# Kernel optimization log

Hardware: AMD Instinct MI355X
Metric: run time of the kernel (lower is better)

Reference implementation:

```python
import jax, jax.numpy as jnp
import numpy as np

N_NODES = 100000
N_HE = 20000
N_INC = 800000
D = 128
HEADS = 4
OUT = D // HEADS  # 32
NEG_SLOPE = 0.2
EPS_GN = 1e-5
EPS_SM = 1e-16


def graph_norm(x, w, b, ms):
    # PyG GraphNorm over a single graph: subtract learnable-scaled mean, normalize by std
    mean = jnp.mean(x, axis=0, keepdims=True)
    xc = x - ms * mean
    var = jnp.mean(xc * xc, axis=0, keepdims=True)
    return w * xc / jnp.sqrt(var + EPS_GN) + b


def frame_update(x, eidx, eattr, W, att, bias):
    # x: [N, D], eidx: [2, E] (row0 node ids, row1 hyperedge ids), eattr: [HE, D]
    xh = (x @ W).reshape(-1, HEADS, OUT)       # [N, H, O]
    eh = (eattr @ W).reshape(-1, HEADS, OUT)   # [HE, H, O]
    src = eidx[0]
    dst = eidx[1]
    x_i = xh[src]                              # [E, H, O] gathered node feats
    x_j = eh[dst]                              # [E, H, O] gathered hyperedge feats
    # attention logit: cat([x_i, x_j]) . att  summed over feature dim
    alpha = jnp.sum(x_i * att[:, :, :OUT], axis=-1) + jnp.sum(x_j * att[:, :, OUT:], axis=-1)  # [E, H]
    alpha = jnp.where(alpha >= 0, alpha, NEG_SLOPE * alpha)  # leaky_relu
    # segment softmax grouped by hyperedge id (dst), num_segments = N_HE
    m = jax.ops.segment_max(alpha, dst, num_segments=N_HE)   # [HE, H]
    ex = jnp.exp(alpha - m[dst])
    s = jax.ops.segment_sum(ex, dst, num_segments=N_HE)      # [HE, H]
    alpha = ex / (s[dst] + EPS_SM)                           # [E, H]
    # message = alpha * x_j where propagate's x_j = x[edge_index[0]] (node feats)
    msg = alpha[:, :, None] * x_i                            # [E, H, O]
    out = jax.ops.segment_sum(msg, dst, num_segments=N_HE)   # [HE, H, O]
    out = out.reshape(-1, HEADS * OUT)                       # concat heads
    return out + bias


def setup_inputs() -> dict:
    key = jax.random.key(0)
    ks = jax.random.split(key, 12)
    g = 1.0 / np.sqrt(D)
    inp = {
        "intra_x": jax.random.normal(ks[0], (N_NODES, D), jnp.float32),
        "intra_edge_attr": jax.random.normal(ks[1], (N_HE, D), jnp.float32),
        "inter_x": jax.random.normal(ks[2], (N_NODES, D), jnp.float32),
        "inter_edge_attr": jax.random.normal(ks[3], (N_HE, D), jnp.float32),
        "intra_edge_index": jnp.stack([
            jax.random.randint(ks[4], (N_INC,), 0, N_NODES),
            jax.random.randint(ks[5], (N_INC,), 0, N_HE)]).astype(jnp.int32),
        "inter_edge_index": jnp.stack([
            jax.random.randint(ks[6], (N_INC,), 0, N_NODES),
            jax.random.randint(ks[7], (N_INC,), 0, N_HE)]).astype(jnp.int32),
        "gn_intra_w": jnp.ones((D,), jnp.float32),
        "gn_intra_b": jnp.zeros((D,), jnp.float32),
        "gn_intra_ms": jnp.ones((D,), jnp.float32),
        "W_intra": jax.random.normal(ks[8], (D, HEADS * OUT), jnp.float32) * g,
        "att_intra": jax.random.normal(ks[9], (1, HEADS, 2 * OUT), jnp.float32) * g,
        "b_intra": jnp.zeros((HEADS * OUT,), jnp.float32),
        "gn_inter_w": jnp.ones((D,), jnp.float32),
        "gn_inter_b": jnp.zeros((D,), jnp.float32),
        "gn_inter_ms": jnp.ones((D,), jnp.float32),
        "W_inter": jax.random.normal(ks[10], (D, HEADS * OUT), jnp.float32) * g,
        "att_inter": jax.random.normal(ks[11], (1, HEADS, 2 * OUT), jnp.float32) * g,
        "b_inter": jnp.zeros((HEADS * OUT,), jnp.float32),
    }
    return inp


def reference(intra_x, intra_edge_index, intra_edge_attr,
              inter_x, inter_edge_index, inter_edge_attr,
              gn_intra_w, gn_intra_b, gn_intra_ms, W_intra, att_intra, b_intra,
              gn_inter_w, gn_inter_b, gn_inter_ms, W_inter, att_inter, b_inter):
    f_intra = frame_update(graph_norm(intra_x, gn_intra_w, gn_intra_b, gn_intra_ms),
                           intra_edge_index, intra_edge_attr, W_intra, att_intra, b_intra)
    f_inter = frame_update(graph_norm(inter_x, gn_inter_w, gn_inter_b, gn_inter_ms),
                           inter_edge_index, inter_edge_attr, W_inter, att_inter, b_inter)
    fusion = jnp.concatenate([
        jnp.mean(f_intra, axis=0),
        jnp.mean(f_inter, axis=0),
        jnp.mean(intra_x, axis=0),
        jnp.mean(inter_x, axis=0),
    ], axis=-1)  # [4*D]
    return fusion
```

## Files before the change

kernel.cpp:

```cpp
#include <hip/hip_runtime.h>

#define N_NODES 100000
#define N_HE    20000
#define N_EDGE  800000
#define DIM     128
#define NBS     98
#define NBD     40
#define CAP_S   9600
#define CAP_D   22500
#define SUBS    8
#define SUBD    16
#define PB      256
#define CHUNK   3125
#define STB     400
#define GPB     512
#define GGRP    32

struct P {
  const void* x[2]; const void* ea[2]; const int* ei[2];
  const void* gw[2]; const void* gb[2]; const void* gms[2];
  const void* W[2]; const void* att[2]; const void* bias[2];
  float *stats, *a, *cw, *v, *u, *cst, *sPart, *wnPart, *gpart, *gpart2;
  unsigned *curS, *curD, *recS, *recD, *done;
  unsigned short *lnb, *lhb, *hsv;
  int* flag; void* out;
};

__device__ __forceinline__ float ldf(const void* p, int i, int isbf){
  if (isbf){ unsigned short h = ((const unsigned short*)p)[i]; return __uint_as_float(((unsigned)h)<<16); }
  return ((const float*)p)[i];
}
__device__ __forceinline__ float b2f(unsigned short h){
  return __uint_as_float(((unsigned)h)<<16);
}
struct F8 { float v[8]; };
__device__ __forceinline__ F8 load8(const void* p, long idx, int isbf){
  F8 r;
  if (isbf){
    uint4 q = *(const uint4*)((const unsigned short*)p + idx);
    r.v[0]=__uint_as_float(q.x<<16); r.v[1]=__uint_as_float(q.x&0xFFFF0000u);
    r.v[2]=__uint_as_float(q.y<<16); r.v[3]=__uint_as_float(q.y&0xFFFF0000u);
    r.v[4]=__uint_as_float(q.z<<16); r.v[5]=__uint_as_float(q.z&0xFFFF0000u);
    r.v[6]=__uint_as_float(q.w<<16); r.v[7]=__uint_as_float(q.w&0xFFFF0000u);
  } else {
    const float4* q = (const float4*)((const float*)p + idx);
    float4 A=q[0], B=q[1];
    r.v[0]=A.x;r.v[1]=A.y;r.v[2]=A.z;r.v[3]=A.w;
    r.v[4]=B.x;r.v[5]=B.y;r.v[6]=B.z;r.v[7]=B.w;
  }
  return r;
}
__device__ __forceinline__ unsigned short f2bf(float f){
  unsigned u = __float_as_uint(f);
  return (unsigned short)((u + 0x7FFFu + ((u>>16)&1u)) >> 16);
}

__global__ void k_detect(P p){
  for (int i=threadIdx.x; i<880; i+=256) p.stats[i]=0.f;
  const unsigned* w = (const unsigned*)p.x[0];
  int bad = 0;
  for (int i = threadIdx.x; i < 4096; i += 256){
    float g = __uint_as_float(w[i]<<16);
    float ag = fabsf(g);
    if (!(ag==0.0f || (ag>1e-8f && ag<1e8f))) bad++;
  }
  for (int o=32;o;o>>=1) bad += __shfl_down(bad,o);
  __shared__ int sb;
  if (threadIdx.x==0) sb=0;
  __syncthreads();
  if ((threadIdx.x&63)==0) atomicAdd(&sb,bad);
  __syncthreads();
  if (threadIdx.x==0) *p.flag = (sb < 512) ? 1 : 0;
}

__global__ __launch_bounds__(256) void k_statsbin(P p){
  __shared__ unsigned smem[6664];
  int t = threadIdx.x;
  if (blockIdx.y < 2){
    int f = blockIdx.y;
    const void* x = p.x[f];
    int isbf = *p.flag;
    int cb = t & 15, rg = t >> 4;
    int rpb = (N_NODES + STB - 1)/STB;
    int r0 = blockIdx.x*rpb;
    int r1 = r0 + rpb; if (r1 > N_NODES) r1 = N_NODES;
    float s[8], q[8];
    #pragma unroll
    for (int j=0;j<8;j++){ s[j]=0.f; q[j]=0.f; }
    for (int r = r0 + rg; r < r1; r += 16){
      F8 xv = load8(x, (long)r*DIM + cb*8, isbf);
      #pragma unroll
      for (int j=0;j<8;j++){ s[j]+=xv.v[j]; q[j]+=xv.v[j]*xv.v[j]; }
    }
    float* red = (float*)smem;
    #pragma unroll
    for (int j=0;j<8;j++) red[t*9+j]=s[j];
    __syncthreads();
    if (t < 128){
      int cb2 = t>>3, j = t&7;
      float a=0.f;
      for (int g=0; g<16; g++) a += red[(g*16+cb2)*9 + j];
      atomicAdd(&p.stats[f*256 + cb2*8 + j], a);
    }
    __syncthreads();
    #pragma unroll
    for (int j=0;j<8;j++) red[t*9+j]=q[j];
    __syncthreads();
    if (t < 128){
      int cb2 = t>>3, j = t&7;
      float a=0.f;
      for (int g=0; g<16; g++) a += red[(g*16+cb2)*9 + j];
      atomicAdd(&p.stats[f*256 + 128 + cb2*8 + j], a);
    }
    return;
  }
  int b = blockIdx.x, f = blockIdx.y - 2;
  if (b >= PB) return;
  unsigned* stage1 = smem;
  unsigned* stage2 = smem + 3125;
  unsigned* histS  = smem + 6250;
  unsigned* histD  = smem + 6348;
  unsigned* startS = smem + 6388;
  unsigned* startD = smem + 6486;
  unsigned* gbaseS = smem + 6526;
  unsigned* gbaseD = smem + 6624;
  const int* ei = p.ei[f];
  if (t < NBS) histS[t]=0;
  if (t < NBD) histD[t]=0;
  __syncthreads();
  int e0 = b*CHUNK;
  for (int i=t; i<CHUNK; i+=256){
    int src = ei[e0+i], dst = ei[N_EDGE+e0+i];
    unsigned nbs = (unsigned)src >> 10;
    stage1[i] = ((unsigned)src & 1023u) | ((unsigned)dst<<10) | (nbs<<25);
    atomicAdd(&histS[nbs], 1u);
    atomicAdd(&histD[(unsigned)dst>>9], 1u);
  }
  __syncthreads();
  if (t==0){ unsigned r=0; for (int k=0;k<NBS;k++){ startS[k]=r; r+=histS[k]; } }
  if (t==1){ unsigned r=0; for (int k=0;k<NBD;k++){ startD[k]=r; r+=histD[k]; } }
  __syncthreads();
  if (t < NBS) gbaseS[t] = atomicAdd(&p.curS[f*NBS+t], histS[t]);
  if (t >= 128 && t < 128+NBD) gbaseD[t-128] = atomicAdd(&p.curD[f*NBD+(t-128)], histD[t-128]);
  __syncthreads();
  if (t < NBS) histS[t]=0;
  __syncthreads();
  for (int i=t; i<CHUNK; i+=256){
    unsigned rec = stage1[i];
    unsigned nbs = rec>>25;
    unsigned r = atomicAdd(&histS[nbs],1u);
    stage2[startS[nbs]+r] = rec;
  }
  __syncthreads();
  for (int i=t; i<CHUNK; i+=256){
    unsigned rec = stage2[i];
    unsigned nbs = rec>>25;
    unsigned g = gbaseS[nbs] + (i - startS[nbs]);
    if (g < CAP_S) p.recS[((long)f*NBS+nbs)*CAP_S + g] = rec & 0x01FFFFFFu;
  }
  __syncthreads();
  if (t < NBD) histD[t]=0;
  __syncthreads();
  for (int i=t; i<CHUNK; i+=256){
    unsigned rec = stage1[i];
    unsigned dst = (rec>>10)&0x7FFFu;
    unsigned src = (rec>>25)*1024u + (rec&1023u);
    unsigned nbd = dst>>9;
    unsigned rd = (dst&511u) | (src<<9) | (nbd<<26);
    unsigned r = atomicAdd(&histD[nbd],1u);
    stage2[startD[nbd]+r] = rd;
  }
  __syncthreads();
  for (int i=t; i<CHUNK; i+=256){
    unsigned rd = stage2[i];
    unsigned nbd = rd>>26;
    unsigned g = gbaseD[nbd] + (i - startD[nbd]);
    if (g < CAP_D) p.recD[((long)f*NBD+nbd)*CAP_D + g] = rd & 0x03FFFFFFu;
  }
}

__global__ void k_prep(P p){
  __shared__ float csh[2][128];
  int t = threadIdx.x;
  int isbf = *p.flag;
  int f = t>>7, d = t&127;
  float sum = p.stats[f*256+d], sq = p.stats[f*256+128+d];
  float mean = sum * (1.0f/N_NODES);
  float ms = ldf(p.gms[f], d, isbf);
  float gw = ldf(p.gw[f],  d, isbf);
  float gb = ldf(p.gb[f],  d, isbf);
  float var = sq*(1.0f/N_NODES) - (2.0f*ms - ms*ms)*mean*mean;
  float av = gw / sqrtf(var + 1e-5f);
  p.a[f*128+d] = av;
  csh[f][d] = gb - av*ms*mean;
  if (isbf) ((unsigned short*)p.out)[256 + f*128 + d] = f2bf(mean);
  else      ((float*)p.out)[256 + f*128 + d] = mean;
  #pragma unroll
  for (int h=0; h<4; h++){
    float w1=0.f, w2=0.f;
    for (int o=0;o<32;o++){
      float Wv = ldf(p.W[f], d*DIM + h*32 + o, isbf);
      w1 += Wv * ldf(p.att[f], h*64+o,    isbf);
      w2 += Wv * ldf(p.att[f], h*64+32+o, isbf);
    }
    p.v[f*512 + d*4 + h] = av*w1;
    p.u[f*512 + d*4 + h] = w2;
  }
  __syncthreads();
  float acc = 0.f;
  for (int dd=0; dd<128; dd++) acc += csh[f][dd]*ldf(p.W[f], dd*DIM+d, isbf);
  p.cw[f*128+d] = acc;
  __syncthreads();
  if (t < 8){
    int ff=t>>2, h=t&3;
    float s2=0.f;
    for (int o=0;o<32;o++) s2 += p.cw[ff*128+h*32+o]*ldf(p.att[ff], h*64+o, isbf);
    p.cst[ff*4+h]=s2;
  }
}

__global__ __launch_bounds__(256) void k_logits(P p){
  int job = blockIdx.y;
  int f = job & 1;
  bool node = job < 2;
  int isbf = *p.flag;
  const void* X = node ? p.x[f] : p.ea[f];
  const float* coef = node ? (p.v + f*512) : (p.u + f*512);
  ushort4* outb = node ? ((ushort4*)p.lnb + (long)f*N_NODES)
                       : ((ushort4*)p.lhb + (long)f*N_HE);
  int R = node ? N_NODES : N_HE;
  int cb = threadIdx.x & 15, rl = threadIdx.x >> 4;
  float cf[8][4];
  #pragma unroll
  for (int j=0;j<8;j++)
    #pragma unroll
    for (int h=0;h<4;h++)
      cf[j][h] = coef[(cb*8+j)*4+h];
  float4 cst4 = make_float4(0.f,0.f,0.f,0.f);
  if (node) cst4 = *(const float4*)(p.cst + f*4);
  int rpb = (R + gridDim.x - 1)/gridDim.x;
  int r0 = blockIdx.x*rpb;
  int r1 = r0+rpb; if (r1>R) r1=R;
  for (int r = r0 + rl; r < r1; r += 16){
    F8 xv = load8(X, (long)r*DIM + cb*8, isbf);
    float a0=0.f,a1=0.f,a2=0.f,a3=0.f;
    #pragma unroll
    for (int j=0;j<8;j++){
      a0 += xv.v[j]*cf[j][0];
      a1 += xv.v[j]*cf[j][1];
      a2 += xv.v[j]*cf[j][2];
      a3 += xv.v[j]*cf[j][3];
    }
    #pragma unroll
    for (int m=1;m<16;m<<=1){
      a0 += __shfl_xor(a0,m);
      a1 += __shfl_xor(a1,m);
      a2 += __shfl_xor(a2,m);
      a3 += __shfl_xor(a3,m);
    }
    if (cb==0){
      ushort4 o;
      o.x = f2bf(a0 + cst4.x);
      o.y = f2bf(a1 + cst4.y);
      o.z = f2bf(a2 + cst4.z);
      o.w = f2bf(a3 + cst4.w);
      outb[r] = o;
    }
  }
}

__global__ __launch_bounds__(256) void k_sD(P p){
  __shared__ float sh[512*4];
  int nbd = blockIdx.x, sub = blockIdx.y, f = blockIdx.z, t = threadIdx.x;
  for (int i=t; i<512; i+=256) *(float4*)(sh+i*4) = make_float4(0,0,0,0);
  __syncthreads();
  unsigned cnt = p.curD[f*NBD+nbd]; if (cnt > CAP_D) cnt = CAP_D;
  int lo = (int)((long)cnt*sub/SUBD), hi = (int)((long)cnt*(sub+1)/SUBD);
  const unsigned* base = p.recD + ((long)f*NBD+nbd)*CAP_D;
  const ushort4* lnb = (const ushort4*)p.lnb + (long)f*N_NODES;
  const ushort4* lhb = (const ushort4*)p.lhb + (long)f*N_HE;
  for (int i=lo+t; i<hi; i+=256){
    unsigned rd = base[i];
    unsigned dstRel = rd & 511u;
    unsigned src = rd >> 9;
    ushort4 A = lnb[src];
    ushort4 B = lhb[nbd*512 + dstRel];
    float z0=b2f(A.x)+b2f(B.x), z1=b2f(A.y)+b2f(B.y);
    float z2=b2f(A.z)+b2f(B.z), z3=b2f(A.w)+b2f(B.w);
    z0 = z0>=0.f? z0 : 0.2f*z0;  z1 = z1>=0.f? z1 : 0.2f*z1;
    z2 = z2>=0.f? z2 : 0.2f*z2;  z3 = z3>=0.f? z3 : 0.2f*z3;
    float* tgt = sh + dstRel*4;
    atomicAdd(tgt+0, __expf(z0));
    atomicAdd(tgt+1, __expf(z1));
    atomicAdd(tgt+2, __expf(z2));
    atomicAdd(tgt+3, __expf(z3));
  }
  __syncthreads();
  float* out = p.sPart + (((long)f*NBD+nbd)*SUBD + sub)*2048;
  for (int i=t; i<512; i+=256) *(float4*)(out+i*4) = *(float4*)(sh+i*4);
}

__global__ void k_sred(P p){
  int idx = blockIdx.x*256 + threadIdx.x;
  if (idx >= 2*N_HE) return;
  int f = idx / N_HE, he = idx % N_HE;
  int nbd = he>>9, rel = he&511;
  float4 acc = make_float4(0,0,0,0);
  const float* base = p.sPart + ((long)(f*NBD+nbd)*SUBD)*2048 + rel*4;
  #pragma unroll
  for (int s=0;s<SUBD;s++){
    float4 v = *(const float4*)(base + (long)s*2048);
    acc.x+=v.x; acc.y+=v.y; acc.z+=v.z; acc.w+=v.w;
  }
  ushort4 lh = ((const ushort4*)p.lhb)[(long)f*N_HE + he];
  uint4 o;
  o.x = (unsigned)lh.x | ((unsigned)lh.y<<16);
  o.y = (unsigned)lh.z | ((unsigned)lh.w<<16);
  o.z = (unsigned)f2bf(1.0f/(acc.x+1e-16f)) | ((unsigned)f2bf(1.0f/(acc.y+1e-16f))<<16);
  o.w = (unsigned)f2bf(1.0f/(acc.z+1e-16f)) | ((unsigned)f2bf(1.0f/(acc.w+1e-16f))<<16);
  ((uint4*)p.hsv)[(long)f*N_HE + he] = o;
}

__global__ __launch_bounds__(256) void k_wnD(P p){
  __shared__ float sh[1024*4];
  int nbs = blockIdx.x, sub = blockIdx.y, f = blockIdx.z, t = threadIdx.x;
  for (int i=t; i<1024; i+=256) *(float4*)(sh+i*4) = make_float4(0,0,0,0);
  __syncthreads();
  unsigned cnt = p.curS[f*NBS+nbs]; if (cnt > CAP_S) cnt = CAP_S;
  int lo = (int)((long)cnt*sub/SUBS), hi = (int)((long)cnt*(sub+1)/SUBS);
  const unsigned* base = p.recS + ((long)f*NBS+nbs)*CAP_S;
  const ushort4* lnb = (const ushort4*)p.lnb + (long)f*N_NODES;
  const uint4* hsv = (const uint4*)p.hsv + (long)f*N_HE;
  for (int i=lo+t; i<hi; i+=256){
    unsigned rec = base[i];
    unsigned srcRel = rec & 1023u;
    unsigned dst = rec >> 10;
    ushort4 A = lnb[nbs*1024 + srcRel];
    uint4 H = hsv[dst];
    float z0=b2f(A.x)+b2f((unsigned short)(H.x&0xFFFF)), z1=b2f(A.y)+b2f((unsigned short)(H.x>>16));
    float z2=b2f(A.z)+b2f((unsigned short)(H.y&0xFFFF)), z3=b2f(A.w)+b2f((unsigned short)(H.y>>16));
    z0 = z0>=0.f? z0 : 0.2f*z0;  z1 = z1>=0.f? z1 : 0.2f*z1;
    z2 = z2>=0.f? z2 : 0.2f*z2;  z3 = z3>=0.f? z3 : 0.2f*z3;
    float si0=b2f((unsigned short)(H.z&0xFFFF)), si1=b2f((unsigned short)(H.z>>16));
    float si2=b2f((unsigned short)(H.w&0xFFFF)), si3=b2f((unsigned short)(H.w>>16));
    float* tgt = sh + srcRel*4;
    atomicAdd(tgt+0, __expf(z0)*si0);
    atomicAdd(tgt+1, __expf(z1)*si1);
    atomicAdd(tgt+2, __expf(z2)*si2);
    atomicAdd(tgt+3, __expf(z3)*si3);
  }
  __syncthreads();
  float* out = p.wnPart + (((long)f*NBS+nbs)*SUBS + sub)*4096;
  for (int i=t; i<1024; i+=256) *(float4*)(out+i*4) = *(float4*)(sh+i*4);
}

__global__ __launch_bounds__(256) void k_gpass(P p){
  int f = blockIdx.y;
  int isbf = *p.flag;
  const void* xs = p.x[f];
  int cb = threadIdx.x & 15, rg = threadIdx.x >> 4;
  float acc[8][4]; float sw[4]={0.f,0.f,0.f,0.f};
  #pragma unroll
  for (int j=0;j<8;j++)
    #pragma unroll
    for (int h=0;h<4;h++) acc[j][h]=0.f;
  int rpb = (N_NODES + gridDim.x - 1)/gridDim.x;
  int r0 = blockIdx.x*rpb;
  int r1 = r0+rpb; if (r1>N_NODES) r1=N_NODES;
  for (int r = r0 + rg; r < r1; r += 16){
    int nbs = r>>10, rel = r&1023;
    const float* wb = p.wnPart + ((long)(f*NBS+nbs)*SUBS)*4096 + rel*4;
    float4 wv = make_float4(0,0,0,0);
    #pragma unroll
    for (int s=0;s<SUBS;s++){
      float4 v = *(const float4*)(wb + (long)s*4096);
      wv.x+=v.x; wv.y+=v.y; wv.z+=v.z; wv.w+=v.w;
    }
    F8 xv = load8(xs, (long)r*DIM + cb*8, isbf);
    float wvv[4]={wv.x,wv.y,wv.z,wv.w};
    #pragma unroll
    for (int j=0;j<8;j++)
      #pragma unroll
      for (int h=0;h<4;h++) acc[j][h] += xv.v[j]*wvv[h];
    if (cb==0){ sw[0]+=wv.x; sw[1]+=wv.y; sw[2]+=wv.z; sw[3]+=wv.w; }
  }
  __shared__ float red[16][16][33];
  __shared__ float red2[16][4];
  #pragma unroll
  for (int j=0;j<8;j++)
    #pragma unroll
    for (int h=0;h<4;h++) red[rg][cb][j*4+h]=acc[j][h];
  if (cb==0){ red2[rg][0]=sw[0]; red2[rg][1]=sw[1]; red2[rg][2]=sw[2]; red2[rg][3]=sw[3]; }
  __syncthreads();
  float* gp = p.gpart + ((long)f*GPB + blockIdx.x)*520;
  for (int idx=threadIdx.x; idx<512; idx+=256){
    int d=idx>>2, h=idx&3, cb2=d>>3, j=d&7;
    float a=0.f;
    #pragma unroll
    for (int g=0; g<16; g++) a += red[g][cb2][j*4+h];
    gp[idx] = a;
  }
  if (threadIdx.x<4){
    float a=0.f;
    for (int g=0;g<16;g++) a+=red2[g][threadIdx.x];
    gp[512+threadIdx.x] = a;
  }
}

__global__ void k_gredfin(P p){
  int g = blockIdx.x, f = blockIdx.y;
  int slabs = GPB/GGRP;
  const float* base = p.gpart + ((long)f*GPB + (long)g*slabs)*520;
  for (int i=threadIdx.x; i<516; i+=256){
    float acc = 0.f;
    for (int s=0;s<slabs;s++) acc += base[(long)s*520 + i];
    p.gpart2[((long)f*GGRP + g)*520 + i] = acc;
  }
  __syncthreads();
  __threadfence();
  __shared__ unsigned isLast;
  if (threadIdx.x==0){
    unsigned old = atomicAdd(p.done, 1u);
    isLast = (old == (unsigned)(GGRP*2 - 1)) ? 1u : 0u;
  }
  __syncthreads();
  if (!isLast) return;
  __threadfence();
  __shared__ float Gs[2][512];
  __shared__ float SWs[2][4];
  int t = threadIdx.x;
  for (int idx=t; idx<2*516; idx+=256){
    int ff = idx/516, i = idx%516;
    const float* b = p.gpart2 + (long)ff*GGRP*520 + i;
    float acc = 0.f;
    for (int gg=0; gg<GGRP; gg++) acc += b[(long)gg*520];
    if (i < 512) Gs[ff][i] = acc; else SWs[ff][i-512] = acc;
  }
  __syncthreads();
  int isbf = *p.flag;
  int ff = t>>7, k = t&127, h = k>>5;
  float acc = 0.f;
  for (int d=0; d<128; d++)
    acc += Gs[ff][d*4+h] * p.a[ff*128+d] * ldf(p.W[ff], d*DIM+k, isbf);
  acc += p.cw[ff*128+k]*SWs[ff][h];
  float o = acc*(1.0f/N_HE) + ldf(p.bias[ff], k, isbf);
  if (isbf) ((unsigned short*)p.out)[ff*128+k] = f2bf(o);
  else      ((float*)p.out)[ff*128+k] = o;
}

extern "C" void kernel_launch(void* const* d_in, const int* in_sizes, int n_in,
                              void* d_out, int out_size, void* d_ws, size_t ws_size,
                              hipStream_t stream){
  P p;
  p.x[0]=d_in[0];  p.ea[0]=d_in[1];  p.x[1]=d_in[2];  p.ea[1]=d_in[3];
  p.ei[0]=(const int*)d_in[4];  p.ei[1]=(const int*)d_in[5];
  p.gw[0]=d_in[6];  p.gb[0]=d_in[7];  p.gms[0]=d_in[8];
  p.W[0]=d_in[9];   p.att[0]=d_in[10]; p.bias[0]=d_in[11];
  p.gw[1]=d_in[12]; p.gb[1]=d_in[13]; p.gms[1]=d_in[14];
  p.W[1]=d_in[15];  p.att[1]=d_in[16]; p.bias[1]=d_in[17];

  float* w = (float*)d_ws;
  size_t off = 0;
  p.stats = w+off; off += 512;
  p.flag  = (int*)(w+off); off += 8;
  p.curS  = (unsigned*)(w+off); off += 256;
  p.curD  = (unsigned*)(w+off); off += 96;
  p.done  = (unsigned*)(w+off); off += 8;
  p.a     = w+off; off += 256;
  p.cw    = w+off; off += 256;
  p.v     = w+off; off += 1024;
  p.u     = w+off; off += 1024;
  p.cst   = w+off; off += 16;
  p.lnb   = (unsigned short*)(w+off); off += (size_t)2*N_NODES*2;
  p.lhb   = (unsigned short*)(w+off); off += (size_t)2*N_HE*2;
  p.hsv   = (unsigned short*)(w+off); off += (size_t)2*N_HE*4;
  p.recS  = (unsigned*)(w+off); off += (size_t)2*NBS*CAP_S;
  p.recD  = (unsigned*)(w+off); off += (size_t)2*NBD*CAP_D;
  p.sPart = w+off; off += (size_t)2*NBD*SUBD*2048;
  p.wnPart= w+off; off += (size_t)2*NBS*SUBS*4096;
  p.gpart = w+off; off += (size_t)2*GPB*520;
  p.gpart2= w+off; off += (size_t)2*GGRP*520;
  p.out   = d_out;

  k_detect  <<<dim3(1),          dim3(256), 0, stream>>>(p);
  k_statsbin<<<dim3(STB,4),      dim3(256), 0, stream>>>(p);
  k_prep    <<<dim3(1),          dim3(256), 0, stream>>>(p);
  k_logits  <<<dim3(STB,4),      dim3(256), 0, stream>>>(p);
  k_sD      <<<dim3(NBD,SUBD,2), dim3(256), 0, stream>>>(p);
  k_sred    <<<dim3((2*N_HE+255)/256), dim3(256), 0, stream>>>(p);
  k_wnD     <<<dim3(NBS,SUBS,2), dim3(256), 0, stream>>>(p);
  k_gpass   <<<dim3(GPB,2),      dim3(256), 0, stream>>>(p);
  k_gredfin <<<dim3(GGRP,2),     dim3(256), 0, stream>>>(p);
}
```

Before: 227.2 us.

## Fuse partial reductions via last-block pattern and add coalesced fp32 streaming paths

```diff
diff --git a/kernel.cpp b/kernel.cpp
--- a/kernel.cpp
+++ b/kernel.cpp
@@ -20,8 +20,8 @@
   const void* x[2]; const void* ea[2]; const int* ei[2];
   const void* gw[2]; const void* gb[2]; const void* gms[2];
   const void* W[2]; const void* att[2]; const void* bias[2];
-  float *stats, *a, *cw, *v, *u, *cst, *sPart, *wnPart, *gpart, *gpart2;
-  unsigned *curS, *curD, *recS, *recD, *done;
+  float *stats, *a, *cw, *v, *u, *cst, *sPart, *wnPart, *wn, *gpart, *gpart2;
+  unsigned *curS, *curD, *done, *sDone, *wDone, *recS, *recD;
   unsigned short *lnb, *lhb, *hsv;
   int* flag; void* out;
 };
@@ -56,7 +56,7 @@
 }
 
 __global__ void k_detect(P p){
-  for (int i=threadIdx.x; i<880; i+=256) p.stats[i]=0.f;
+  for (int i=threadIdx.x; i<1200; i+=256) p.stats[i]=0.f;
   const unsigned* w = (const unsigned*)p.x[0];
   int bad = 0;
   for (int i = threadIdx.x; i < 4096; i += 256){
@@ -78,8 +78,39 @@
   int t = threadIdx.x;
   if (blockIdx.y < 2){
     int f = blockIdx.y;
+    int isbf = *p.flag;
+    if (!isbf){
+      const float4* xf = (const float4*)p.x[f];
+      const long NF4 = (long)N_NODES*32;
+      const long G = (long)STB*256;
+      long i0 = (long)blockIdx.x*256 + t;
+      float s0=0,s1=0,s2=0,s3=0,q0=0,q1=0,q2=0,q3=0;
+      for (long i=i0; i<NF4; i+=G){
+        float4 v = xf[i];
+        s0+=v.x; q0+=v.x*v.x; s1+=v.y; q1+=v.y*v.y;
+        s2+=v.z; q2+=v.z*v.z; s3+=v.w; q3+=v.w*v.w;
+      }
+      s0 += __shfl_xor(s0,32); q0 += __shfl_xor(q0,32);
+      s1 += __shfl_xor(s1,32); q1 += __shfl_xor(q1,32);
+      s2 += __shfl_xor(s2,32); q2 += __shfl_xor(q2,32);
+      s3 += __shfl_xor(s3,32); q3 += __shfl_xor(q3,32);
+      float* redf = (float*)smem;
+      int wave=t>>6, lane=t&63;
+      if (lane<32){
+        float* d = redf + (wave*32+lane)*8;
+        d[0]=s0; d[1]=s1; d[2]=s2; d[3]=s3; d[4]=q0; d[5]=q1; d[6]=q2; d[7]=q3;
+      }
+      __syncthreads();
+      if (t < 128){
+        int g = t>>2, k = t&3;
+        float a = redf[(0*32+g)*8+k]+redf[(1*32+g)*8+k]+redf[(2*32+g)*8+k]+redf[(3*32+g)*8+k];
+        float aq= redf[(0*32+g)*8+4+k]+redf[(1*32+g)*8+4+k]+redf[(2*32+g)*8+4+k]+redf[(3*32+g)*8+4+k];
+        atomicAdd(&p.stats[f*256 + t], a);
+        atomicAdd(&p.stats[f*256 + 128 + t], aq);
+      }
+      return;
+    }
     const void* x = p.x[f];
-    int isbf = *p.flag;
     int cb = t & 15, rg = t >> 4;
     int rpb = (N_NODES + STB - 1)/STB;
     int r0 = blockIdx.x*rpb;
@@ -88,7 +119,7 @@
     #pragma unroll
     for (int j=0;j<8;j++){ s[j]=0.f; q[j]=0.f; }
     for (int r = r0 + rg; r < r1; r += 16){
-      F8 xv = load8(x, (long)r*DIM + cb*8, isbf);
+      F8 xv = load8(x, (long)r*DIM + cb*8, 1);
       #pragma unroll
       for (int j=0;j<8;j++){ s[j]+=xv.v[j]; q[j]+=xv.v[j]*xv.v[j]; }
     }
@@ -229,20 +260,58 @@
   ushort4* outb = node ? ((ushort4*)p.lnb + (long)f*N_NODES)
                        : ((ushort4*)p.lhb + (long)f*N_HE);
   int R = node ? N_NODES : N_HE;
-  int cb = threadIdx.x & 15, rl = threadIdx.x >> 4;
+  int t = threadIdx.x;
+  float4 cst4 = make_float4(0.f,0.f,0.f,0.f);
+  if (node) cst4 = *(const float4*)(p.cst + f*4);
+  if (!isbf){
+    int c = t & 31;
+    float cf[4][4];
+    #pragma unroll
+    for (int k=0;k<4;k++)
+      #pragma unroll
+      for (int h=0;h<4;h++)
+        cf[k][h] = coef[(c*4+k)*4+h];
+    const float4* Xf = (const float4*)X;
+    const long NF4 = (long)R*32;
+    const long G = (long)gridDim.x*256;
+    long i0 = (long)blockIdx.x*256 + t;
+    for (long i=i0; i<NF4; i+=G){
+      float4 v = Xf[i];
+      float p0 = v.x*cf[0][0]+v.y*cf[1][0]+v.z*cf[2][0]+v.w*cf[3][0];
+      float p1 = v.x*cf[0][1]+v.y*cf[1][1]+v.z*cf[2][1]+v.w*cf[3][1];
+      float p2 = v.x*cf[0][2]+v.y*cf[1][2]+v.z*cf[2][2]+v.w*cf[3][2];
+      float p3 = v.x*cf[0][3]+v.y*cf[1][3]+v.z*cf[2][3]+v.w*cf[3][3];
+      #pragma unroll
+      for (int m=1;m<32;m<<=1){
+        p0 += __shfl_xor(p0,m);
+        p1 += __shfl_xor(p1,m);
+        p2 += __shfl_xor(p2,m);
+        p3 += __shfl_xor(p3,m);
+      }
+      if (c==0){
+        long row = i >> 5;
+        ushort4 o;
+        o.x = f2bf(p0 + cst4.x);
+        o.y = f2bf(p1 + cst4.y);
+        o.z = f2bf(p2 + cst4.z);
+        o.w = f2bf(p3 + cst4.w);
+        outb[row] = o;
+      }
+    }
+    return;
+  }
+  int cb = t & 15, rl = t >> 4;
   float cf[8][4];
   #pragma unroll
   for (int j=0;j<8;j++)
     #pragma unroll
     for (int h=0;h<4;h++)
       cf[j][h] = coef[(cb*8+j)*4+h];
-  float4 cst4 = make_float4(0.f,0.f,0.f,0.f);
-  if (node) cst4 = *(const float4*)(p.cst + f*4);
   int rpb = (R + gridDim.x - 1)/gridDim.x;
   int r0 = blockIdx.x*rpb;
   int r1 = r0+rpb; if (r1>R) r1=R;
   for (int r = r0 + rl; r < r1; r += 16){
-    F8 xv = load8(X, (long)r*DIM + cb*8, isbf);
+    F8 xv = load8(X, (long)r*DIM + cb*8, 1);
     float a0=0.f,a1=0.f,a2=0.f,a3=0.f;
     #pragma unroll
     for (int j=0;j<8;j++){
@@ -298,27 +367,30 @@
   __syncthreads();
   float* out = p.sPart + (((long)f*NBD+nbd)*SUBD + sub)*2048;
   for (int i=t; i<512; i+=256) *(float4*)(out+i*4) = *(float4*)(sh+i*4);
-}
-
-__global__ void k_sred(P p){
-  int idx = blockIdx.x*256 + threadIdx.x;
-  if (idx >= 2*N_HE) return;
-  int f = idx / N_HE, he = idx % N_HE;
-  int nbd = he>>9, rel = he&511;
-  float4 acc = make_float4(0,0,0,0);
-  const float* base = p.sPart + ((long)(f*NBD+nbd)*SUBD)*2048 + rel*4;
-  #pragma unroll
-  for (int s=0;s<SUBD;s++){
-    float4 v = *(const float4*)(base + (long)s*2048);
-    acc.x+=v.x; acc.y+=v.y; acc.z+=v.z; acc.w+=v.w;
-  }
-  ushort4 lh = ((const ushort4*)p.lhb)[(long)f*N_HE + he];
-  uint4 o;
-  o.x = (unsigned)lh.x | ((unsigned)lh.y<<16);
-  o.y = (unsigned)lh.z | ((unsigned)lh.w<<16);
-  o.z = (unsigned)f2bf(1.0f/(acc.x+1e-16f)) | ((unsigned)f2bf(1.0f/(acc.y+1e-16f))<<16);
-  o.w = (unsigned)f2bf(1.0f/(acc.z+1e-16f)) | ((unsigned)f2bf(1.0f/(acc.w+1e-16f))<<16);
-  ((uint4*)p.hsv)[(long)f*N_HE + he] = o;
+  __threadfence();
+  __shared__ unsigned isLast;
+  if (t==0) isLast = (atomicAdd(&p.sDone[f*NBD+nbd],1u) == SUBD-1) ? 1u : 0u;
+  __syncthreads();
+  if (!isLast) return;
+  __threadfence();
+  const float* pb = p.sPart + ((long)(f*NBD+nbd)*SUBD)*2048;
+  for (int rel=t; rel<512; rel+=256){
+    int he = nbd*512 + rel;
+    if (he >= N_HE) continue;
+    float4 acc = make_float4(0,0,0,0);
+    #pragma unroll
+    for (int s=0;s<SUBD;s++){
+      float4 v = *(const float4*)(pb + (long)s*2048 + rel*4);
+      acc.x+=v.x; acc.y+=v.y; acc.z+=v.z; acc.w+=v.w;
+    }
+    ushort4 lh = lhb[he];
+    uint4 o;
+    o.x = (unsigned)lh.x | ((unsigned)lh.y<<16);
+    o.y = (unsigned)lh.z | ((unsigned)lh.w<<16);
+    o.z = (unsigned)f2bf(1.0f/(acc.x+1e-16f)) | ((unsigned)f2bf(1.0f/(acc.y+1e-16f))<<16);
+    o.w = (unsigned)f2bf(1.0f/(acc.z+1e-16f)) | ((unsigned)f2bf(1.0f/(acc.w+1e-16f))<<16);
+    ((uint4*)p.hsv)[(long)f*N_HE + he] = o;
+  }
 }
 
 __global__ __launch_bounds__(256) void k_wnD(P p){
@@ -352,58 +424,117 @@
   __syncthreads();
   float* out = p.wnPart + (((long)f*NBS+nbs)*SUBS + sub)*4096;
   for (int i=t; i<1024; i+=256) *(float4*)(out+i*4) = *(float4*)(sh+i*4);
+  __threadfence();
+  __shared__ unsigned isLast;
+  if (t==0) isLast = (atomicAdd(&p.wDone[f*NBS+nbs],1u) == SUBS-1) ? 1u : 0u;
+  __syncthreads();
+  if (!isLast) return;
+  __threadfence();
+  const float* pb = p.wnPart + ((long)(f*NBS+nbs)*SUBS)*4096;
+  for (int rel=t; rel<1024; rel+=256){
+    int node = nbs*1024 + rel;
+    if (node >= N_NODES) continue;
+    float4 acc = make_float4(0,0,0,0);
+    #pragma unroll
+    for (int s=0;s<SUBS;s++){
+      float4 v = *(const float4*)(pb + (long)s*4096 + rel*4);
+      acc.x+=v.x; acc.y+=v.y; acc.z+=v.z; acc.w+=v.w;
+    }
+    ((float4*)p.wn)[(long)f*N_NODES + node] = acc;
+  }
 }
 
 __global__ __launch_bounds__(256) void k_gpass(P p){
   int f = blockIdx.y;
   int isbf = *p.flag;
+  int t = threadIdx.x;
+  __shared__ float red[4][32][16];
+  __shared__ float red2[4][4];
+  float acc[4][4];
+  #pragma unroll
+  for (int k=0;k<4;k++)
+    #pragma unroll
+    for (int h=0;h<4;h++) acc[k][h]=0.f;
+  float sw[4]={0.f,0.f,0.f,0.f};
+  int wave=t>>6, lane=t&63;
+  if (!isbf){
+    const float4* xf = (const float4*)p.x[f];
+    const float4* wnf = (const float4*)p.wn + (long)f*N_NODES;
+    const long NF4 = (long)N_NODES*32;
+    const long G = (long)GPB*256;
+    long i0 = (long)blockIdx.x*256 + t;
+    int c = t & 31;
+    for (long i=i0; i<NF4; i+=G){
+      float4 xv = xf[i];
+      float4 wv = wnf[i>>5];
+      acc[0][0]+=xv.x*wv.x; acc[0][1]+=xv.x*wv.y; acc[0][2]+=xv.x*wv.z; acc[0][3]+=xv.x*wv.w;
+      acc[1][0]+=xv.y*wv.x; acc[1][1]+=xv.y*wv.y; acc[1][2]+=xv.y*wv.z; acc[1][3]+=xv.y*wv.w;
+      acc[2][0]+=xv.z*wv.x; acc[2][1]+=xv.z*wv.y; acc[2][2]+=xv.z*wv.z; acc[2][3]+=xv.z*wv.w;
+      acc[3][0]+=xv.w*wv.x; acc[3][1]+=xv.w*wv.y; acc[3][2]+=xv.w*wv.z; acc[3][3]+=xv.w*wv.w;
+      if (c==0){ sw[0]+=wv.x; sw[1]+=wv.y; sw[2]+=wv.z; sw[3]+=wv.w; }
+    }
+    #pragma unroll
+    for (int k=0;k<4;k++)
+      #pragma unroll
+      for (int h=0;h<4;h++) acc[k][h] += __shfl_xor(acc[k][h], 32);
+    #pragma unroll
+    for (int h=0;h<4;h++) sw[h] += __shfl_xor(sw[h], 32);
+    if (lane<32){
+      #pragma unroll
+      for (int k=0;k<4;k++)
+        #pragma unroll
+        for (int h=0;h<4;h++) red[wave][lane][k*4+h]=acc[k][h];
+    }
+    if (lane==0){ red2[wave][0]=sw[0]; red2[wave][1]=sw[1]; red2[wave][2]=sw[2]; red2[wave][3]=sw[3]; }
+    __syncthreads();
+    float* gp = p.gpart + ((long)f*GPB + blockIdx.x)*520;
+    for (int idx=t; idx<512; idx+=256){
+      int d=idx>>2, h=idx&3, g=d>>2, k=d&3;
+      gp[idx] = red[0][g][k*4+h]+red[1][g][k*4+h]+red[2][g][k*4+h]+red[3][g][k*4+h];
+    }
+    if (t<4) gp[512+t] = red2[0][t]+red2[1][t]+red2[2][t]+red2[3][t];
+    return;
+  }
   const void* xs = p.x[f];
-  int cb = threadIdx.x & 15, rg = threadIdx.x >> 4;
-  float acc[8][4]; float sw[4]={0.f,0.f,0.f,0.f};
+  int cb = t & 15, rg = t >> 4;
+  float accb[8][4]; float swb[4]={0.f,0.f,0.f,0.f};
   #pragma unroll
   for (int j=0;j<8;j++)
     #pragma unroll
-    for (int h=0;h<4;h++) acc[j][h]=0.f;
-  int rpb = (N_NODES + gridDim.x - 1)/gridDim.x;
+    for (int h=0;h<4;h++) accb[j][h]=0.f;
+  int rpb = (N_NODES + GPB - 1)/GPB;
   int r0 = blockIdx.x*rpb;
   int r1 = r0+rpb; if (r1>N_NODES) r1=N_NODES;
   for (int r = r0 + rg; r < r1; r += 16){
-    int nbs = r>>10, rel = r&1023;
-    const float* wb = p.wnPart + ((long)(f*NBS+nbs)*SUBS)*4096 + rel*4;
-    float4 wv = make_float4(0,0,0,0);
-    #pragma unroll
-    for (int s=0;s<SUBS;s++){
-      float4 v = *(const float4*)(wb + (long)s*4096);
-      wv.x+=v.x; wv.y+=v.y; wv.z+=v.z; wv.w+=v.w;
-    }
-    F8 xv = load8(xs, (long)r*DIM + cb*8, isbf);
+    float4 wv = *(const float4*)(p.wn + ((long)f*N_NODES + r)*4);
+    F8 xv = load8(xs, (long)r*DIM + cb*8, 1);
     float wvv[4]={wv.x,wv.y,wv.z,wv.w};
     #pragma unroll
     for (int j=0;j<8;j++)
       #pragma unroll
-      for (int h=0;h<4;h++) acc[j][h] += xv.v[j]*wvv[h];
-    if (cb==0){ sw[0]+=wv.x; sw[1]+=wv.y; sw[2]+=wv.z; sw[3]+=wv.w; }
-  }
-  __shared__ float red[16][16][33];
-  __shared__ float red2[16][4];
+      for (int h=0;h<4;h++) accb[j][h] += xv.v[j]*wvv[h];
+    if (cb==0){ swb[0]+=wv.x; swb[1]+=wv.y; swb[2]+=wv.z; swb[3]+=wv.w; }
+  }
+  __shared__ float redb[16][16][33];
+  __shared__ float redb2[16][4];
   #pragma unroll
   for (int j=0;j<8;j++)
     #pragma unroll
-    for (int h=0;h<4;h++) red[rg][cb][j*4+h]=acc[j][h];
-  if (cb==0){ red2[rg][0]=sw[0]; red2[rg][1]=sw[1]; red2[rg][2]=sw[2]; red2[rg][3]=sw[3]; }
+    for (int h=0;h<4;h++) redb[rg][cb][j*4+h]=accb[j][h];
+  if (cb==0){ redb2[rg][0]=swb[0]; redb2[rg][1]=swb[1]; redb2[rg][2]=swb[2]; redb2[rg][3]=swb[3]; }
   __syncthreads();
   float* gp = p.gpart + ((long)f*GPB + blockIdx.x)*520;
-  for (int idx=threadIdx.x; idx<512; idx+=256){
+  for (int idx=t; idx<512; idx+=256){
     int d=idx>>2, h=idx&3, cb2=d>>3, j=d&7;
     float a=0.f;
     #pragma unroll
-    for (int g=0; g<16; g++) a += red[g][cb2][j*4+h];
+    for (int g=0; g<16; g++) a += redb[g][cb2][j*4+h];
     gp[idx] = a;
   }
-  if (threadIdx.x<4){
+  if (t<4){
     float a=0.f;
-    for (int g=0;g<16;g++) a+=red2[g][threadIdx.x];
-    gp[512+threadIdx.x] = a;
+    for (int g=0;g<16;g++) a+=redb2[g][t];
+    gp[512+t] = a;
   }
 }
 
@@ -466,6 +597,8 @@
   p.curS  = (unsigned*)(w+off); off += 256;
   p.curD  = (unsigned*)(w+off); off += 96;
   p.done  = (unsigned*)(w+off); off += 8;
+  p.sDone = (unsigned*)(w+off); off += 96;
+  p.wDone = (unsigned*)(w+off); off += 224;
   p.a     = w+off; off += 256;
   p.cw    = w+off; off += 256;
   p.v     = w+off; off += 1024;
@@ -478,6 +611,7 @@
   p.recD  = (unsigned*)(w+off); off += (size_t)2*NBD*CAP_D;
   p.sPart = w+off; off += (size_t)2*NBD*SUBD*2048;
   p.wnPart= w+off; off += (size_t)2*NBS*SUBS*4096;
+  p.wn    = w+off; off += (size_t)2*N_NODES*4;
   p.gpart = w+off; off += (size_t)2*GPB*520;
   p.gpart2= w+off; off += (size_t)2*GGRP*520;
   p.out   = d_out;
@@ -487,7 +621,6 @@
   k_prep    <<<dim3(1),          dim3(256), 0, stream>>>(p);
   k_logits  <<<dim3(STB,4),      dim3(256), 0, stream>>>(p);
   k_sD      <<<dim3(NBD,SUBD,2), dim3(256), 0, stream>>>(p);
-  k_sred    <<<dim3((2*N_HE+255)/256), dim3(256), 0, stream>>>(p);
   k_wnD     <<<dim3(NBS,SUBS,2), dim3(256), 0, stream>>>(p);
   k_gpass   <<<dim3(GPB,2),      dim3(256), 0, stream>>>(p);
   k_gredfin <<<dim3(GGRP,2),     dim3(256), 0, stream>>>(p);
```

After: 532.2 us. 134% more time.
